# Kernel tuning notes

Hardware: AMD Instinct MI355X
Metric: run time of the kernel (lower is better)

Reference implementation:

```python
import jax, jax.numpy as jnp
import numpy as np

MAX_CH = 21
LAT_DIM = 64
D_EMBED = 1024
N_HEADS = 16
D_HEAD = D_EMBED // N_HEADS  # 64
L = MAX_CH * LAT_DIM         # 1344 latents
B, T = 4, 1024


def setup_inputs() -> dict:
    key = jax.random.key(0)
    k1, k2, k3, k4, k5, k6 = jax.random.split(key, 6)
    x = jax.random.normal(k1, (B, T, D_EMBED), dtype=jnp.float32)
    # boolean channel mask [b, L, T]
    ch_mask = jax.random.randint(k2, (B, L, T), 0, 2) > 0
    # learned latent queries [L, H*d] (xavier-uniform-ish init)
    lim_q = float(np.sqrt(6.0 / (L + N_HEADS * D_HEAD)))
    latent_q = jax.random.uniform(k3, (L, N_HEADS * D_HEAD), minval=-lim_q, maxval=lim_q, dtype=jnp.float32)
    # Linear weights (torch layout: [out, in]) and biases
    lim_w = float(np.sqrt(1.0 / D_EMBED))
    w_k_w = jax.random.uniform(k4, (N_HEADS * D_HEAD, D_EMBED), minval=-lim_w, maxval=lim_w, dtype=jnp.float32)
    w_k_b = jnp.zeros((N_HEADS * D_HEAD,), dtype=jnp.float32)
    w_v_w = jax.random.uniform(k5, (N_HEADS * D_HEAD, D_EMBED), minval=-lim_w, maxval=lim_w, dtype=jnp.float32)
    w_v_b = jax.random.uniform(k6, (N_HEADS * D_HEAD,), minval=-lim_w, maxval=lim_w, dtype=jnp.float32)
    return {"x": x, "ch_mask": ch_mask, "latent_q": latent_q,
            "w_k_w": w_k_w, "w_k_b": w_k_b, "w_v_w": w_v_w, "w_v_b": w_v_b}


def reference(x, ch_mask, latent_q, w_k_w, w_k_b, w_v_w, w_v_b):
    b, t, d = x.shape
    H, dh = N_HEADS, D_HEAD
    l = latent_q.shape[0]
    # faithful to torch .view(-1, H, L, d): raw row-major reinterpretation
    lq = latent_q.reshape(1, H, l, dh)                    # [1,H,L,dh]
    k = (x @ w_k_w.T + w_k_b).reshape(b, t, H, dh).transpose(0, 2, 3, 1)  # [b,H,dh,T]
    v = (x @ w_v_w.T + w_v_b).reshape(b, t, H, dh).transpose(0, 2, 1, 3)  # [b,H,T,dh]
    scale = jnp.float32(H) ** -0.5  # note: n_heads**-0.5, as in source
    scores = jnp.einsum('ohld,bhdt->bhlt', lq, k) * scale  # [b,H,L,T]
    mask = ch_mask[:, None, :, :]                           # [b,1,L,T] broadcast over heads
    scores = jnp.where(mask, scores, jnp.float32(-1e9))
    w = jax.nn.softmax(scores, axis=-1)
    w = jnp.where(mask, w, jnp.float32(0.0))
    out = jnp.einsum('bhlt,bhtd->bhld', w, v)               # [b,H,L,dh]
    return out.transpose(0, 2, 1, 3).reshape(b, l, H * dh)  # [b,L,H*dh]
```

## Files before the change

### kernel.cpp

```cpp
#include <hip/hip_runtime.h>
#include <hip/hip_bf16.h>

#define B_SZ 4
#define T_SZ 1024
#define NH 16
#define L_SZ 1344
#define LT_COUNT 21

typedef __attribute__((ext_vector_type(8))) short short8;
typedef __attribute__((ext_vector_type(4))) short short4v;
typedef __attribute__((ext_vector_type(4))) float floatx4;

typedef __attribute__((address_space(1))) const void gvoid;
typedef __attribute__((address_space(3))) void svoid;
#define GLD16(gp, lp) \
  __builtin_amdgcn_global_load_lds((gvoid*)(gp), (svoid*)(lp), 16, 0, 0)

static __device__ inline short bf16bits(float f) {
  return __builtin_bit_cast(short, __float2bfloat16(f));
}
static __device__ inline short4v cvt4(float4 v) {
  short4v r;
  r.x = bf16bits(v.x); r.y = bf16bits(v.y);
  r.z = bf16bits(v.z); r.w = bf16bits(v.w);
  return r;
}

static __device__ inline void store_kv(int gn, int grow, float val,
    __hip_bfloat16* __restrict__ k_buf, __hip_bfloat16* __restrict__ v_buf) {
  int b = grow >> 10, t = grow & 1023;
  if (gn < 1024) {
    int h = gn >> 6, d = gn & 63;
    int bh = b * 16 + h;
    int tc = t >> 6, ni = (t >> 4) & 3, c15 = t & 15;
    int half = (d >> 5) & 1, q4 = (d >> 3) & 3, jj = d & 7;
    k_buf[(size_t)((bh * 16 + tc) * 8 + ni * 2 + half) * 512 +
          (q4 * 16 + c15) * 8 + jj] = __float2bfloat16(val);
  } else {
    int dd = gn - 1024;
    int h = dd >> 6, d = dd & 63;
    int bh = b * 16 + h;
    int tc = t >> 6, half = (t >> 5) & 1, q4 = (t >> 3) & 3, jj = t & 7;
    int di = (d >> 4) & 3, c15 = d & 15;
    v_buf[(size_t)((bh * 16 + tc) * 8 + di * 2 + half) * 512 +
          (q4 * 16 + c15) * 8 + jj] = __float2bfloat16(val);
  }
}

__global__ __launch_bounds__(256) void mask_detect(
    const unsigned char* __restrict__ m, int* __restrict__ flag) {
  __shared__ int any_off4, any_at4;
  if (threadIdx.x == 0) { any_off4 = 0; any_at4 = 0; }
  __syncthreads();
  int a1 = 0, a2 = 0;
  for (int i = threadIdx.x; i < 8192; i += 256) {
    unsigned char v = m[i];
    if (v) {
      if ((i & 3) != 0) a1 = 1;
      if ((i & 7) == 4) a2 = 1;
    }
  }
  if (a1) atomicOr(&any_off4, 1);
  if (a2) atomicOr(&any_at4, 1);
  __syncthreads();
  if (threadIdx.x == 0) *flag = any_off4 ? 1 : (any_at4 ? 0 : 2);
}

__global__ __launch_bounds__(256) void maskbits_kernel(
    const void* __restrict__ mask, const int* __restrict__ flag,
    unsigned int* __restrict__ bits) {
  int idx = blockIdx.x * 256 + threadIdx.x;
  int f = *flag;
  bool v;
  if (f == 1)      v = ((const signed char*)mask)[idx] != 0;
  else if (f == 2) v = ((const long long*)mask)[idx] != 0;
  else             v = ((const int*)mask)[idx] != 0;
  unsigned long long bal = __ballot(v);
  int lane = threadIdx.x & 63;
  if ((lane & 31) == 0) {
    unsigned int w = (lane & 32) ? (unsigned int)(bal >> 32) : (unsigned int)bal;
    bits[idx >> 5] = w;
  }
}

__global__ __launch_bounds__(256) void cvt_bf16(
    const float4* __restrict__ src, short4v* __restrict__ dst) {
  size_t i = (size_t)blockIdx.x * 256 + threadIdx.x;
  dst[i] = cvt4(src[i]);
}

__global__ __launch_bounds__(256) void kv_gemm_bf16(
    const __hip_bfloat16* __restrict__ xb,
    const __hip_bfloat16* __restrict__ wb,
    const float* __restrict__ bk, const float* __restrict__ bv,
    __hip_bfloat16* __restrict__ k_buf, __hip_bfloat16* __restrict__ v_buf) {
  __shared__ __align__(16) __hip_bfloat16 ldsA[128 * 32];
  __shared__ __align__(16) __hip_bfloat16 ldsB[128 * 32];

  const int tid = threadIdx.x, lane = tid & 63, w = tid >> 6;
  const int wm = w & 1, wn = w >> 1;
  const int bx = blockIdx.x, by = blockIdx.y;
  const int c15 = lane & 15, kq = lane >> 4;

  floatx4 acc[4][4];
  for (int i = 0; i < 4; ++i)
    for (int j = 0; j < 4; ++j) acc[i][j] = (floatx4){0.f, 0.f, 0.f, 0.f};

  for (int kk = 0; kk < 1024; kk += 32) {
    #pragma unroll
    for (int j = 0; j < 2; ++j) {
      int c = w * 128 + j * 64 + lane;
      int row = c >> 2;
      int gkc = (c & 3) ^ (row & 3);
      GLD16(xb + (size_t)(by * 128 + row) * 1024 + kk + gkc * 8,
            ldsA + (w * 128 + j * 64) * 8);
      GLD16(wb + (size_t)(bx * 128 + row) * 1024 + kk + gkc * 8,
            ldsB + (w * 128 + j * 64) * 8);
    }
    __syncthreads();

    short8 af[4], bf[4];
    #pragma unroll
    for (int mi = 0; mi < 4; ++mi) {
      int row = wm * 64 + mi * 16 + c15;
      af[mi] = *(const short8*)(ldsA + row * 32 + ((kq ^ (row & 3)) * 8));
    }
    #pragma unroll
    for (int ni = 0; ni < 4; ++ni) {
      int row = wn * 64 + ni * 16 + c15;
      bf[ni] = *(const short8*)(ldsB + row * 32 + ((kq ^ (row & 3)) * 8));
    }
    #pragma unroll
    for (int mi = 0; mi < 4; ++mi)
      #pragma unroll
      for (int ni = 0; ni < 4; ++ni)
        acc[mi][ni] = __builtin_amdgcn_mfma_f32_16x16x32_bf16(af[mi], bf[ni], acc[mi][ni], 0, 0, 0);
    __syncthreads();
  }

  #pragma unroll
  for (int ni = 0; ni < 4; ++ni) {
    int gn = bx * 128 + wn * 64 + ni * 16 + c15;
    float bias = (gn < 1024) ? bk[gn] : bv[gn - 1024];
    #pragma unroll
    for (int mi = 0; mi < 4; ++mi) {
      int grow0 = by * 128 + wm * 64 + mi * 16 + (kq << 2);
      #pragma unroll
      for (int r = 0; r < 4; ++r)
        store_kv(gn, grow0 + r, acc[mi][ni][r] + bias, k_buf, v_buf);
    }
  }
}

__global__ __launch_bounds__(256) void kv_gemm_f32(
    const float* __restrict__ x,
    const float* __restrict__ wk, const float* __restrict__ bk,
    const float* __restrict__ wv, const float* __restrict__ bv,
    __hip_bfloat16* __restrict__ k_buf, __hip_bfloat16* __restrict__ v_buf) {
  __shared__ __align__(16) __hip_bfloat16 ldsA[128 * 40];
  __shared__ __align__(16) __hip_bfloat16 ldsB[128 * 40];
  const int tid = threadIdx.x, lane = tid & 63, w = tid >> 6;
  const int wm = w & 1, wn = w >> 1;
  const int bx = blockIdx.x, by = blockIdx.y;
  const bool isK = (bx < 8);
  const float* W = isK ? wk : wv;
  const int n0 = bx * 128 - (isK ? 0 : 1024);
  floatx4 acc[4][4];
  for (int i = 0; i < 4; ++i)
    for (int j = 0; j < 4; ++j) acc[i][j] = (floatx4){0.f, 0.f, 0.f, 0.f};
  const int c15 = lane & 15, kq = lane >> 4;
  for (int kk = 0; kk < 1024; kk += 32) {
    #pragma unroll
    for (int j = 0; j < 4; ++j) {
      int f = tid + 256 * j;
      int row = f >> 3, c4 = (f & 7) * 4;
      float4 va = *(const float4*)(x + (size_t)(by * 128 + row) * 1024 + kk + c4);
      float4 vb = *(const float4*)(W + (size_t)(n0 + row) * 1024 + kk + c4);
      *(short4v*)(ldsA + row * 40 + c4) = cvt4(va);
      *(short4v*)(ldsB + row * 40 + c4) = cvt4(vb);
    }
    __syncthreads();
    short8 af[4], bf[4];
    #pragma unroll
    for (int mi = 0; mi < 4; ++mi)
      af[mi] = *(const short8*)(ldsA + (wm * 64 + mi * 16 + c15) * 40 + kq * 8);
    #pragma unroll
    for (int ni = 0; ni < 4; ++ni)
      bf[ni] = *(const short8*)(ldsB + (wn * 64 + ni * 16 + c15) * 40 + kq * 8);
    #pragma unroll
    for (int mi = 0; mi < 4; ++mi)
      #pragma unroll
      for (int ni = 0; ni < 4; ++ni)
        acc[mi][ni] = __builtin_amdgcn_mfma_f32_16x16x32_bf16(af[mi], bf[ni], acc[mi][ni], 0, 0, 0);
    __syncthreads();
  }
  #pragma unroll
  for (int ni = 0; ni < 4; ++ni) {
    int gn = bx * 128 + wn * 64 + ni * 16 + c15;
    float bias = (gn < 1024) ? bk[gn] : bv[gn - 1024];
    #pragma unroll
    for (int mi = 0; mi < 4; ++mi) {
      int grow0 = by * 128 + wm * 64 + mi * 16 + (kq << 2);
      #pragma unroll
      for (int r = 0; r < 4; ++r)
        store_kv(gn, grow0 + r, acc[mi][ni][r] + bias, k_buf, v_buf);
    }
  }
}

__global__ __launch_bounds__(64, 4) void attn_kernel(
    const float* __restrict__ latent_q,
    const __hip_bfloat16* __restrict__ k_buf,
    const __hip_bfloat16* __restrict__ v_buf,
    const unsigned int* __restrict__ mbits,
    float* __restrict__ out) {
  __shared__ __align__(16) __hip_bfloat16 pbuf[2][16 * 72];

  const int lane = threadIdx.x & 63;
  int bid = blockIdx.x;
  int xcd = bid & 7, j = bid >> 3;
  int bh = xcd * 8 + j / 84;
  int r84 = j % 84;
  int lt = r84 >> 2, sub = r84 & 3;
  int h = bh & 15, b = bh >> 4;
  const int q4 = lane >> 4, c15 = lane & 15;
  const int l = lt * 64 + sub * 16 + c15;

  const float QS = 0.25f * 1.44269504089f;
  short8 qf[2];
  {
    const float* qp = latent_q + ((size_t)(h * L_SZ + l)) * 64 + q4 * 8;
    float4 a0 = *(const float4*)(qp);
    float4 a1 = *(const float4*)(qp + 4);
    float4 a2 = *(const float4*)(qp + 32);
    float4 a3 = *(const float4*)(qp + 36);
    a0.x *= QS; a0.y *= QS; a0.z *= QS; a0.w *= QS;
    a1.x *= QS; a1.y *= QS; a1.z *= QS; a1.w *= QS;
    a2.x *= QS; a2.y *= QS; a2.z *= QS; a2.w *= QS;
    a3.x *= QS; a3.y *= QS; a3.z *= QS; a3.w *= QS;
    short4v l0 = cvt4(a0), l1 = cvt4(a1), l2 = cvt4(a2), l3 = cvt4(a3);
    qf[0] = (short8){l0.x, l0.y, l0.z, l0.w, l1.x, l1.y, l1.z, l1.w};
    qf[1] = (short8){l2.x, l2.y, l2.z, l2.w, l3.x, l3.y, l3.z, l3.w};
  }

  float l_acc = 0.f;
  floatx4 o_acc[4];
  #pragma unroll
  for (int di = 0; di < 4; ++di) o_acc[di] = (floatx4){0.f, 0.f, 0.f, 0.f};

  const __hip_bfloat16* kb = k_buf + (size_t)bh * 16 * 4096;
  const __hip_bfloat16* vb = v_buf + (size_t)bh * 16 * 4096;
  const unsigned int* mrow = mbits + ((size_t)(b * L_SZ + l)) * 32;

  for (int tc = 0; tc < 16; ++tc) {
    short8 kf[2][4];
    #pragma unroll
    for (int half = 0; half < 2; ++half)
      #pragma unroll
      for (int ni = 0; ni < 4; ++ni)
        kf[half][ni] = *(const short8*)(kb + (size_t)(tc * 8 + ni * 2 + half) * 512 + lane * 8);
    uint2 mw = *(const uint2*)(mrow + tc * 2);

    floatx4 s[4];
    #pragma unroll
    for (int ni = 0; ni < 4; ++ni) s[ni] = (floatx4){0.f, 0.f, 0.f, 0.f};
    #pragma unroll
    for (int half = 0; half < 2; ++half)
      #pragma unroll
      for (int ni = 0; ni < 4; ++ni)
        s[ni] = __builtin_amdgcn_mfma_f32_16x16x32_bf16(kf[half][ni], qf[half], s[ni], 0, 0, 0);

    short8 vf[2][4];
    #pragma unroll
    for (int half = 0; half < 2; ++half)
      #pragma unroll
      for (int di = 0; di < 4; ++di)
        vf[half][di] = *(const short8*)(vb + (size_t)(tc * 8 + di * 2 + half) * 512 + lane * 8);

    __hip_bfloat16* pw = pbuf[tc & 1];
    #pragma unroll
    for (int ni = 0; ni < 4; ++ni) {
      unsigned mword = (ni >= 2) ? mw.y : mw.x;
      float4 p4;
      #pragma unroll
      for (int r = 0; r < 4; ++r) {
        float e = exp2f(s[ni][r]);
        int sh = (ni & 1) * 16 + q4 * 4 + r;
        float pv = ((mword >> sh) & 1) ? e : 0.f;
        l_acc += pv;
        ((float*)&p4)[r] = pv;
      }
      *(short4v*)(pw + c15 * 72 + ni * 16 + q4 * 4) = cvt4(p4);
    }

    short8 pf0 = *(const short8*)(pw + c15 * 72 + q4 * 8);
    short8 pf1 = *(const short8*)(pw + c15 * 72 + 32 + q4 * 8);

    #pragma unroll
    for (int di = 0; di < 4; ++di)
      o_acc[di] = __builtin_amdgcn_mfma_f32_16x16x32_bf16(vf[0][di], pf0, o_acc[di], 0, 0, 0);
    #pragma unroll
    for (int di = 0; di < 4; ++di)
      o_acc[di] = __builtin_amdgcn_mfma_f32_16x16x32_bf16(vf[1][di], pf1, o_acc[di], 0, 0, 0);
  }

  l_acc += __shfl_xor(l_acc, 16, 64);
  l_acc += __shfl_xor(l_acc, 32, 64);
  float inv = (l_acc > 0.f) ? 1.f / l_acc : 0.f;
  float* ob = out + ((size_t)(b * L_SZ + l)) * 1024 + h * 64;
  #pragma unroll
  for (int di = 0; di < 4; ++di) {
    float4 o4 = {o_acc[di][0] * inv, o_acc[di][1] * inv,
                 o_acc[di][2] * inv, o_acc[di][3] * inv};
    *(float4*)(ob + di * 16 + q4 * 4) = o4;
  }
}

extern "C" void kernel_launch(void* const* d_in, const int* in_sizes, int n_in,
                              void* d_out, int out_size, void* d_ws, size_t ws_size,
                              hipStream_t stream) {
  const float* x      = (const float*)d_in[0];
  const void* ch_mask = d_in[1];
  const float* lq     = (const float*)d_in[2];
  const float* wk     = (const float*)d_in[3];
  const float* bk     = (const float*)d_in[4];
  const float* wv     = (const float*)d_in[5];
  const float* bv     = (const float*)d_in[6];
  float* out = (float*)d_out;

  char* ws = (char*)d_ws;
  unsigned int* mbits   = (unsigned int*)ws;
  int* flag             = (int*)(ws + (992u * 1024));
  __hip_bfloat16* k_buf = (__hip_bfloat16*)(ws + (1u << 20));
  __hip_bfloat16* v_buf = (__hip_bfloat16*)(ws + (9u << 20));
  __hip_bfloat16* xb    = (__hip_bfloat16*)(ws + (17u << 20));
  __hip_bfloat16* wb    = (__hip_bfloat16*)(ws + (25u << 20));

  mask_detect<<<1, 256, 0, stream>>>((const unsigned char*)ch_mask, flag);
  maskbits_kernel<<<21504, 256, 0, stream>>>(ch_mask, flag, mbits);

  if (ws_size >= (30u << 20)) {
    cvt_bf16<<<4096, 256, 0, stream>>>((const float4*)x, (short4v*)xb);
    cvt_bf16<<<1024, 256, 0, stream>>>((const float4*)wk, (short4v*)wb);
    cvt_bf16<<<1024, 256, 0, stream>>>((const float4*)wv,
                                       (short4v*)(wb + 1024 * 1024));
    kv_gemm_bf16<<<dim3(16, 32), 256, 0, stream>>>(xb, wb, bk, bv, k_buf, v_buf);
  } else {
    kv_gemm_f32<<<dim3(16, 32), 256, 0, stream>>>(x, wk, bk, wv, bv, k_buf, v_buf);
  }

  attn_kernel<<<8 * 672, 64, 0, stream>>>(lq, k_buf, v_buf, mbits, out);
}
```

Baseline: 218.4 us.

## Process 64 latents per attention wave and split K/V GEMMs with vectorized epilogues

The attention kernel now handles four 16-latent groups per wavefront, so each K/V fragment load from global memory serves four score/PV MFMA sets. The mask words for the tile are staged in LDS up front. The fused KV GEMM is split into separate K and V GEMMs. K is computed transposed (W·xᵀ) so the epilogue writes contiguous 4-element bf16 vectors in the swizzled layout instead of scattered scalar stores. The trade-off is higher register pressure (launch bounds drop to 2 waves), a quarter as many attention blocks, and one more kernel launch.

```diff
diff --git a/kernel.cpp b/kernel.cpp
--- a/kernel.cpp
+++ b/kernel.cpp
@@ -26,26 +26,6 @@
   return r;
 }
 
-static __device__ inline void store_kv(int gn, int grow, float val,
-    __hip_bfloat16* __restrict__ k_buf, __hip_bfloat16* __restrict__ v_buf) {
-  int b = grow >> 10, t = grow & 1023;
-  if (gn < 1024) {
-    int h = gn >> 6, d = gn & 63;
-    int bh = b * 16 + h;
-    int tc = t >> 6, ni = (t >> 4) & 3, c15 = t & 15;
-    int half = (d >> 5) & 1, q4 = (d >> 3) & 3, jj = d & 7;
-    k_buf[(size_t)((bh * 16 + tc) * 8 + ni * 2 + half) * 512 +
-          (q4 * 16 + c15) * 8 + jj] = __float2bfloat16(val);
-  } else {
-    int dd = gn - 1024;
-    int h = dd >> 6, d = dd & 63;
-    int bh = b * 16 + h;
-    int tc = t >> 6, half = (t >> 5) & 1, q4 = (t >> 3) & 3, jj = t & 7;
-    int di = (d >> 4) & 3, c15 = d & 15;
-    v_buf[(size_t)((bh * 16 + tc) * 8 + di * 2 + half) * 512 +
-          (q4 * 16 + c15) * 8 + jj] = __float2bfloat16(val);
-  }
-}
 
 __global__ __launch_bounds__(256) void mask_detect(
     const unsigned char* __restrict__ m, int* __restrict__ flag) {
@@ -89,147 +69,193 @@
   dst[i] = cvt4(src[i]);
 }
 
-__global__ __launch_bounds__(256) void kv_gemm_bf16(
-    const __hip_bfloat16* __restrict__ xb,
-    const __hip_bfloat16* __restrict__ wb,
-    const float* __restrict__ bk, const float* __restrict__ bv,
-    __hip_bfloat16* __restrict__ k_buf, __hip_bfloat16* __restrict__ v_buf) {
-  __shared__ __align__(16) __hip_bfloat16 ldsA[128 * 32];
-  __shared__ __align__(16) __hip_bfloat16 ldsB[128 * 32];
-
-  const int tid = threadIdx.x, lane = tid & 63, w = tid >> 6;
-  const int wm = w & 1, wn = w >> 1;
-  const int bx = blockIdx.x, by = blockIdx.y;
-  const int c15 = lane & 15, kq = lane >> 4;
-
-  floatx4 acc[4][4];
-  for (int i = 0; i < 4; ++i)
-    for (int j = 0; j < 4; ++j) acc[i][j] = (floatx4){0.f, 0.f, 0.f, 0.f};
-
-  for (int kk = 0; kk < 1024; kk += 32) {
-    #pragma unroll
-    for (int j = 0; j < 2; ++j) {
-      int c = w * 128 + j * 64 + lane;
-      int row = c >> 2;
-      int gkc = (c & 3) ^ (row & 3);
-      GLD16(xb + (size_t)(by * 128 + row) * 1024 + kk + gkc * 8,
-            ldsA + (w * 128 + j * 64) * 8);
-      GLD16(wb + (size_t)(bx * 128 + row) * 1024 + kk + gkc * 8,
-            ldsB + (w * 128 + j * 64) * 8);
-    }
-    __syncthreads();
-
-    short8 af[4], bf[4];
+static __device__ inline void epi_k(const floatx4 acc[4][4],
+    int bx, int by, int wm, int wn, int c15, int kq,
+    const float* __restrict__ bk, __hip_bfloat16* __restrict__ k_buf) {
+  #pragma unroll
+  for (int ni = 0; ni < 4; ++ni) {
+    int gr = bx * 128 + wn * 64 + ni * 16 + c15;
+    int b = gr >> 10, tc = (gr >> 6) & 15;
     #pragma unroll
     for (int mi = 0; mi < 4; ++mi) {
-      int row = wm * 64 + mi * 16 + c15;
-      af[mi] = *(const short8*)(ldsA + row * 32 + ((kq ^ (row & 3)) * 8));
-    }
-    #pragma unroll
-    for (int ni = 0; ni < 4; ++ni) {
-      int row = wn * 64 + ni * 16 + c15;
-      bf[ni] = *(const short8*)(ldsB + row * 32 + ((kq ^ (row & 3)) * 8));
-    }
-    #pragma unroll
-    for (int mi = 0; mi < 4; ++mi)
-      #pragma unroll
-      for (int ni = 0; ni < 4; ++ni)
-        acc[mi][ni] = __builtin_amdgcn_mfma_f32_16x16x32_bf16(af[mi], bf[ni], acc[mi][ni], 0, 0, 0);
-    __syncthreads();
-  }
-
+      int d0 = by * 128 + wm * 64 + mi * 16 + kq * 4;
+      int h = d0 >> 6, hd = d0 & 63;
+      int half = hd >> 5, q4 = (hd >> 3) & 3, jlo = hd & 7;
+      int bh = b * 16 + h;
+      float4 b4 = *(const float4*)(bk + d0);
+      float4 v4 = {acc[mi][ni][0] + b4.x, acc[mi][ni][1] + b4.y,
+                   acc[mi][ni][2] + b4.z, acc[mi][ni][3] + b4.w};
+      *(short4v*)(k_buf + ((size_t)((bh * 16 + tc) * 8 + ni * 2 + half)) * 512 +
+                  (q4 * 16 + c15) * 8 + jlo) = cvt4(v4);
+    }
+  }
+}
+
+static __device__ inline void epi_v(const floatx4 acc[4][4],
+    int bx, int by, int wm, int wn, int c15, int kq,
+    const float* __restrict__ bv, __hip_bfloat16* __restrict__ v_buf) {
   #pragma unroll
   for (int ni = 0; ni < 4; ++ni) {
-    int gn = bx * 128 + wn * 64 + ni * 16 + c15;
-    float bias = (gn < 1024) ? bk[gn] : bv[gn - 1024];
+    int d = bx * 128 + wn * 64 + ni * 16 + c15;
+    int h = d >> 6;
+    float bias = bv[d];
     #pragma unroll
     for (int mi = 0; mi < 4; ++mi) {
-      int grow0 = by * 128 + wm * 64 + mi * 16 + (kq << 2);
-      #pragma unroll
-      for (int r = 0; r < 4; ++r)
-        store_kv(gn, grow0 + r, acc[mi][ni][r] + bias, k_buf, v_buf);
-    }
-  }
-}
-
-__global__ __launch_bounds__(256) void kv_gemm_f32(
-    const float* __restrict__ x,
-    const float* __restrict__ wk, const float* __restrict__ bk,
-    const float* __restrict__ wv, const float* __restrict__ bv,
-    __hip_bfloat16* __restrict__ k_buf, __hip_bfloat16* __restrict__ v_buf) {
-  __shared__ __align__(16) __hip_bfloat16 ldsA[128 * 40];
-  __shared__ __align__(16) __hip_bfloat16 ldsB[128 * 40];
-  const int tid = threadIdx.x, lane = tid & 63, w = tid >> 6;
-  const int wm = w & 1, wn = w >> 1;
-  const int bx = blockIdx.x, by = blockIdx.y;
-  const bool isK = (bx < 8);
-  const float* W = isK ? wk : wv;
-  const int n0 = bx * 128 - (isK ? 0 : 1024);
-  floatx4 acc[4][4];
-  for (int i = 0; i < 4; ++i)
-    for (int j = 0; j < 4; ++j) acc[i][j] = (floatx4){0.f, 0.f, 0.f, 0.f};
-  const int c15 = lane & 15, kq = lane >> 4;
-  for (int kk = 0; kk < 1024; kk += 32) {
-    #pragma unroll
-    for (int j = 0; j < 4; ++j) {
-      int f = tid + 256 * j;
-      int row = f >> 3, c4 = (f & 7) * 4;
-      float4 va = *(const float4*)(x + (size_t)(by * 128 + row) * 1024 + kk + c4);
-      float4 vb = *(const float4*)(W + (size_t)(n0 + row) * 1024 + kk + c4);
-      *(short4v*)(ldsA + row * 40 + c4) = cvt4(va);
-      *(short4v*)(ldsB + row * 40 + c4) = cvt4(vb);
-    }
-    __syncthreads();
-    short8 af[4], bf[4];
-    #pragma unroll
-    for (int mi = 0; mi < 4; ++mi)
-      af[mi] = *(const short8*)(ldsA + (wm * 64 + mi * 16 + c15) * 40 + kq * 8);
-    #pragma unroll
-    for (int ni = 0; ni < 4; ++ni)
-      bf[ni] = *(const short8*)(ldsB + (wn * 64 + ni * 16 + c15) * 40 + kq * 8);
-    #pragma unroll
-    for (int mi = 0; mi < 4; ++mi)
-      #pragma unroll
-      for (int ni = 0; ni < 4; ++ni)
-        acc[mi][ni] = __builtin_amdgcn_mfma_f32_16x16x32_bf16(af[mi], bf[ni], acc[mi][ni], 0, 0, 0);
-    __syncthreads();
-  }
-  #pragma unroll
-  for (int ni = 0; ni < 4; ++ni) {
-    int gn = bx * 128 + wn * 64 + ni * 16 + c15;
-    float bias = (gn < 1024) ? bk[gn] : bv[gn - 1024];
-    #pragma unroll
-    for (int mi = 0; mi < 4; ++mi) {
-      int grow0 = by * 128 + wm * 64 + mi * 16 + (kq << 2);
-      #pragma unroll
-      for (int r = 0; r < 4; ++r)
-        store_kv(gn, grow0 + r, acc[mi][ni][r] + bias, k_buf, v_buf);
-    }
-  }
-}
-
-__global__ __launch_bounds__(64, 4) void attn_kernel(
+      int gr = by * 128 + wm * 64 + mi * 16 + kq * 4;
+      int b = gr >> 10, tc = (gr >> 6) & 15;
+      int tl = gr & 63;
+      int half = tl >> 5, q4 = (tl >> 3) & 3, jlo = tl & 7;
+      int bh = b * 16 + h;
+      float4 v4 = {acc[mi][ni][0] + bias, acc[mi][ni][1] + bias,
+                   acc[mi][ni][2] + bias, acc[mi][ni][3] + bias};
+      *(short4v*)(v_buf + ((size_t)((bh * 16 + tc) * 8 + ni * 2 + half)) * 512 +
+                  (q4 * 16 + c15) * 8 + jlo) = cvt4(v4);
+    }
+  }
+}
+
+#define GEMM_BF16_CORE(Abase, Bbase)                                          \
+  __shared__ __align__(16) __hip_bfloat16 ldsA[128 * 32];                     \
+  __shared__ __align__(16) __hip_bfloat16 ldsB[128 * 32];                     \
+  const int tid = threadIdx.x, lane = tid & 63, w = tid >> 6;                 \
+  const int wm = w & 1, wn = w >> 1;                                          \
+  const int bx = blockIdx.x, by = blockIdx.y;                                 \
+  const int c15 = lane & 15, kq = lane >> 4;                                  \
+  floatx4 acc[4][4];                                                          \
+  for (int i = 0; i < 4; ++i)                                                 \
+    for (int j = 0; j < 4; ++j) acc[i][j] = (floatx4){0.f, 0.f, 0.f, 0.f};    \
+  for (int kk = 0; kk < 1024; kk += 32) {                                     \
+    _Pragma("unroll")                                                         \
+    for (int j = 0; j < 2; ++j) {                                             \
+      int c = w * 128 + j * 64 + lane;                                        \
+      int row = c >> 2;                                                       \
+      int gkc = (c & 3) ^ (row & 3);                                          \
+      GLD16(Abase + (size_t)(by * 128 + row) * 1024 + kk + gkc * 8,           \
+            ldsA + (w * 128 + j * 64) * 8);                                   \
+      GLD16(Bbase + (size_t)(bx * 128 + row) * 1024 + kk + gkc * 8,           \
+            ldsB + (w * 128 + j * 64) * 8);                                   \
+    }                                                                         \
+    __syncthreads();                                                          \
+    short8 af[4], bf[4];                                                      \
+    _Pragma("unroll")                                                         \
+    for (int mi = 0; mi < 4; ++mi) {                                          \
+      int row = wm * 64 + mi * 16 + c15;                                      \
+      af[mi] = *(const short8*)(ldsA + row * 32 + ((kq ^ (row & 3)) * 8));    \
+    }                                                                         \
+    _Pragma("unroll")                                                         \
+    for (int ni = 0; ni < 4; ++ni) {                                          \
+      int row = wn * 64 + ni * 16 + c15;                                      \
+      bf[ni] = *(const short8*)(ldsB + row * 32 + ((kq ^ (row & 3)) * 8));    \
+    }                                                                         \
+    _Pragma("unroll")                                                         \
+    for (int mi = 0; mi < 4; ++mi)                                            \
+      _Pragma("unroll")                                                       \
+      for (int ni = 0; ni < 4; ++ni)                                          \
+        acc[mi][ni] = __builtin_amdgcn_mfma_f32_16x16x32_bf16(                \
+            af[mi], bf[ni], acc[mi][ni], 0, 0, 0);                            \
+    __syncthreads();                                                          \
+  }
+
+__global__ __launch_bounds__(256) void gemm_k_bf16(
+    const __hip_bfloat16* __restrict__ wkb, const __hip_bfloat16* __restrict__ xb,
+    const float* __restrict__ bk, __hip_bfloat16* __restrict__ k_buf) {
+  GEMM_BF16_CORE(wkb, xb)
+  epi_k(acc, bx, by, wm, wn, c15, kq, bk, k_buf);
+}
+
+__global__ __launch_bounds__(256) void gemm_v_bf16(
+    const __hip_bfloat16* __restrict__ xb, const __hip_bfloat16* __restrict__ wvb,
+    const float* __restrict__ bv, __hip_bfloat16* __restrict__ v_buf) {
+  GEMM_BF16_CORE(xb, wvb)
+  epi_v(acc, bx, by, wm, wn, c15, kq, bv, v_buf);
+}
+
+#define GEMM_F32_CORE(Abase, Bbase)                                           \
+  __shared__ __align__(16) __hip_bfloat16 ldsA[128 * 40];                     \
+  __shared__ __align__(16) __hip_bfloat16 ldsB[128 * 40];                     \
+  const int tid = threadIdx.x, lane = tid & 63, w = tid >> 6;                 \
+  const int wm = w & 1, wn = w >> 1;                                          \
+  const int bx = blockIdx.x, by = blockIdx.y;                                 \
+  const int c15 = lane & 15, kq = lane >> 4;                                  \
+  floatx4 acc[4][4];                                                          \
+  for (int i = 0; i < 4; ++i)                                                 \
+    for (int j = 0; j < 4; ++j) acc[i][j] = (floatx4){0.f, 0.f, 0.f, 0.f};    \
+  for (int kk = 0; kk < 1024; kk += 32) {                                     \
+    _Pragma("unroll")                                                         \
+    for (int j = 0; j < 4; ++j) {                                             \
+      int f = tid + 256 * j;                                                  \
+      int row = f >> 3, c4 = (f & 7) * 4;                                     \
+      float4 va = *(const float4*)(Abase + (size_t)(by * 128 + row) * 1024 + kk + c4); \
+      float4 vb = *(const float4*)(Bbase + (size_t)(bx * 128 + row) * 1024 + kk + c4); \
+      *(short4v*)(ldsA + row * 40 + c4) = cvt4(va);                           \
+      *(short4v*)(ldsB + row * 40 + c4) = cvt4(vb);                           \
+    }                                                                         \
+    __syncthreads();                                                          \
+    short8 af[4], bf[4];                                                      \
+    _Pragma("unroll")                                                         \
+    for (int mi = 0; mi < 4; ++mi)                                            \
+      af[mi] = *(const short8*)(ldsA + (wm * 64 + mi * 16 + c15) * 40 + kq * 8); \
+    _Pragma("unroll")                                                         \
+    for (int ni = 0; ni < 4; ++ni)                                            \
+      bf[ni] = *(const short8*)(ldsB + (wn * 64 + ni * 16 + c15) * 40 + kq * 8); \
+    _Pragma("unroll")                                                         \
+    for (int mi = 0; mi < 4; ++mi)                                            \
+      _Pragma("unroll")                                                       \
+      for (int ni = 0; ni < 4; ++ni)                                          \
+        acc[mi][ni] = __builtin_amdgcn_mfma_f32_16x16x32_bf16(                \
+            af[mi], bf[ni], acc[mi][ni], 0, 0, 0);                            \
+    __syncthreads();                                                          \
+  }
+
+__global__ __launch_bounds__(256) void gemm_k_f32(
+    const float* __restrict__ wk, const float* __restrict__ x,
+    const float* __restrict__ bk, __hip_bfloat16* __restrict__ k_buf) {
+  GEMM_F32_CORE(wk, x)
+  epi_k(acc, bx, by, wm, wn, c15, kq, bk, k_buf);
+}
+
+__global__ __launch_bounds__(256) void gemm_v_f32(
+    const float* __restrict__ x, const float* __restrict__ wv,
+    const float* __restrict__ bv, __hip_bfloat16* __restrict__ v_buf) {
+  GEMM_F32_CORE(x, wv)
+  epi_v(acc, bx, by, wm, wn, c15, kq, bv, v_buf);
+}
+
+__global__ __launch_bounds__(64, 2) void attn_kernel(
     const float* __restrict__ latent_q,
     const __hip_bfloat16* __restrict__ k_buf,
     const __hip_bfloat16* __restrict__ v_buf,
     const unsigned int* __restrict__ mbits,
     float* __restrict__ out) {
-  __shared__ __align__(16) __hip_bfloat16 pbuf[2][16 * 72];
+  __shared__ __align__(16) __hip_bfloat16 pbuf[4][16 * 72];
+  __shared__ uint2 mrows[64][17];
 
   const int lane = threadIdx.x & 63;
   int bid = blockIdx.x;
   int xcd = bid & 7, j = bid >> 3;
-  int bh = xcd * 8 + j / 84;
-  int r84 = j % 84;
-  int lt = r84 >> 2, sub = r84 & 3;
+  int bh = xcd * 8 + j / LT_COUNT;
+  int lt = j % LT_COUNT;
   int h = bh & 15, b = bh >> 4;
   const int q4 = lane >> 4, c15 = lane & 15;
-  const int l = lt * 64 + sub * 16 + c15;
+  const int l0 = lt * 64;
+
+  {
+    const unsigned int* msrc = mbits + (size_t)(b * L_SZ + l0) * 32;
+    #pragma unroll
+    for (int p = 0; p < 8; ++p) {
+      int i = p * 64 + lane;
+      uint4 m4 = *(const uint4*)(msrc + i * 4);
+      int row = i >> 3, c2 = (i & 7) * 2;
+      mrows[row][c2]     = make_uint2(m4.x, m4.y);
+      mrows[row][c2 + 1] = make_uint2(m4.z, m4.w);
+    }
+  }
 
   const float QS = 0.25f * 1.44269504089f;
-  short8 qf[2];
-  {
-    const float* qp = latent_q + ((size_t)(h * L_SZ + l)) * 64 + q4 * 8;
+  short8 qf[4][2];
+  #pragma unroll
+  for (int g = 0; g < 4; ++g) {
+    const float* qp = latent_q + ((size_t)(h * L_SZ + l0 + g * 16 + c15)) * 64 + q4 * 8;
     float4 a0 = *(const float4*)(qp);
     float4 a1 = *(const float4*)(qp + 4);
     float4 a2 = *(const float4*)(qp + 32);
@@ -238,81 +264,88 @@
     a1.x *= QS; a1.y *= QS; a1.z *= QS; a1.w *= QS;
     a2.x *= QS; a2.y *= QS; a2.z *= QS; a2.w *= QS;
     a3.x *= QS; a3.y *= QS; a3.z *= QS; a3.w *= QS;
-    short4v l0 = cvt4(a0), l1 = cvt4(a1), l2 = cvt4(a2), l3 = cvt4(a3);
-    qf[0] = (short8){l0.x, l0.y, l0.z, l0.w, l1.x, l1.y, l1.z, l1.w};
-    qf[1] = (short8){l2.x, l2.y, l2.z, l2.w, l3.x, l3.y, l3.z, l3.w};
-  }
-
-  float l_acc = 0.f;
-  floatx4 o_acc[4];
-  #pragma unroll
-  for (int di = 0; di < 4; ++di) o_acc[di] = (floatx4){0.f, 0.f, 0.f, 0.f};
-
-  const __hip_bfloat16* kb = k_buf + (size_t)bh * 16 * 4096;
-  const __hip_bfloat16* vb = v_buf + (size_t)bh * 16 * 4096;
-  const unsigned int* mrow = mbits + ((size_t)(b * L_SZ + l)) * 32;
+    short4v t0 = cvt4(a0), t1 = cvt4(a1), t2 = cvt4(a2), t3 = cvt4(a3);
+    qf[g][0] = (short8){t0.x, t0.y, t0.z, t0.w, t1.x, t1.y, t1.z, t1.w};
+    qf[g][1] = (short8){t2.x, t2.y, t2.z, t2.w, t3.x, t3.y, t3.z, t3.w};
+  }
+
+  float l_acc[4] = {0.f, 0.f, 0.f, 0.f};
+  floatx4 o_acc[4][4];
+  #pragma unroll
+  for (int g = 0; g < 4; ++g)
+    #pragma unroll
+    for (int di = 0; di < 4; ++di) o_acc[g][di] = (floatx4){0.f, 0.f, 0.f, 0.f};
+
+  const __hip_bfloat16* kb = k_buf + (size_t)bh * 65536;
+  const __hip_bfloat16* vb = v_buf + (size_t)bh * 65536;
 
   for (int tc = 0; tc < 16; ++tc) {
-    short8 kf[2][4];
+    short8 kf[2][4], vf[2][4];
     #pragma unroll
     for (int half = 0; half < 2; ++half)
       #pragma unroll
       for (int ni = 0; ni < 4; ++ni)
         kf[half][ni] = *(const short8*)(kb + (size_t)(tc * 8 + ni * 2 + half) * 512 + lane * 8);
-    uint2 mw = *(const uint2*)(mrow + tc * 2);
-
-    floatx4 s[4];
-    #pragma unroll
-    for (int ni = 0; ni < 4; ++ni) s[ni] = (floatx4){0.f, 0.f, 0.f, 0.f};
-    #pragma unroll
-    for (int half = 0; half < 2; ++half)
-      #pragma unroll
-      for (int ni = 0; ni < 4; ++ni)
-        s[ni] = __builtin_amdgcn_mfma_f32_16x16x32_bf16(kf[half][ni], qf[half], s[ni], 0, 0, 0);
-
-    short8 vf[2][4];
     #pragma unroll
     for (int half = 0; half < 2; ++half)
       #pragma unroll
       for (int di = 0; di < 4; ++di)
         vf[half][di] = *(const short8*)(vb + (size_t)(tc * 8 + di * 2 + half) * 512 + lane * 8);
 
-    __hip_bfloat16* pw = pbuf[tc & 1];
-    #pragma unroll
-    for (int ni = 0; ni < 4; ++ni) {
-      unsigned mword = (ni >= 2) ? mw.y : mw.x;
-      float4 p4;
-      #pragma unroll
-      for (int r = 0; r < 4; ++r) {
-        float e = exp2f(s[ni][r]);
-        int sh = (ni & 1) * 16 + q4 * 4 + r;
-        float pv = ((mword >> sh) & 1) ? e : 0.f;
-        l_acc += pv;
-        ((float*)&p4)[r] = pv;
+    #pragma unroll
+    for (int g = 0; g < 4; ++g) {
+      uint2 mw = mrows[g * 16 + c15][tc];
+      floatx4 s[4];
+      #pragma unroll
+      for (int ni = 0; ni < 4; ++ni) s[ni] = (floatx4){0.f, 0.f, 0.f, 0.f};
+      #pragma unroll
+      for (int half = 0; half < 2; ++half)
+        #pragma unroll
+        for (int ni = 0; ni < 4; ++ni)
+          s[ni] = __builtin_amdgcn_mfma_f32_16x16x32_bf16(kf[half][ni], qf[g][half], s[ni], 0, 0, 0);
+      __hip_bfloat16* pw = pbuf[g];
+      #pragma unroll
+      for (int ni = 0; ni < 4; ++ni) {
+        unsigned mword = (ni >= 2) ? mw.y : mw.x;
+        float4 p4;
+        #pragma unroll
+        for (int r = 0; r < 4; ++r) {
+          float e = exp2f(s[ni][r]);
+          int sh = (ni & 1) * 16 + q4 * 4 + r;
+          float pv = ((mword >> sh) & 1) ? e : 0.f;
+          l_acc[g] += pv;
+          ((float*)&p4)[r] = pv;
+        }
+        *(short4v*)(pw + c15 * 72 + ni * 16 + q4 * 4) = cvt4(p4);
       }
-      *(short4v*)(pw + c15 * 72 + ni * 16 + q4 * 4) = cvt4(p4);
-    }
-
-    short8 pf0 = *(const short8*)(pw + c15 * 72 + q4 * 8);
-    short8 pf1 = *(const short8*)(pw + c15 * 72 + 32 + q4 * 8);
-
-    #pragma unroll
-    for (int di = 0; di < 4; ++di)
-      o_acc[di] = __builtin_amdgcn_mfma_f32_16x16x32_bf16(vf[0][di], pf0, o_acc[di], 0, 0, 0);
-    #pragma unroll
-    for (int di = 0; di < 4; ++di)
-      o_acc[di] = __builtin_amdgcn_mfma_f32_16x16x32_bf16(vf[1][di], pf1, o_acc[di], 0, 0, 0);
-  }
-
-  l_acc += __shfl_xor(l_acc, 16, 64);
-  l_acc += __shfl_xor(l_acc, 32, 64);
-  float inv = (l_acc > 0.f) ? 1.f / l_acc : 0.f;
-  float* ob = out + ((size_t)(b * L_SZ + l)) * 1024 + h * 64;
-  #pragma unroll
-  for (int di = 0; di < 4; ++di) {
-    float4 o4 = {o_acc[di][0] * inv, o_acc[di][1] * inv,
-                 o_acc[di][2] * inv, o_acc[di][3] * inv};
-    *(float4*)(ob + di * 16 + q4 * 4) = o4;
+    }
+
+    #pragma unroll
+    for (int g = 0; g < 4; ++g) {
+      short8 pf0 = *(const short8*)(pbuf[g] + c15 * 72 + q4 * 8);
+      short8 pf1 = *(const short8*)(pbuf[g] + c15 * 72 + 32 + q4 * 8);
+      #pragma unroll
+      for (int di = 0; di < 4; ++di)
+        o_acc[g][di] = __builtin_amdgcn_mfma_f32_16x16x32_bf16(vf[0][di], pf0, o_acc[g][di], 0, 0, 0);
+      #pragma unroll
+      for (int di = 0; di < 4; ++di)
+        o_acc[g][di] = __builtin_amdgcn_mfma_f32_16x16x32_bf16(vf[1][di], pf1, o_acc[g][di], 0, 0, 0);
+    }
+  }
+
+  #pragma unroll
+  for (int g = 0; g < 4; ++g) {
+    float la = l_acc[g];
+    la += __shfl_xor(la, 16, 64);
+    la += __shfl_xor(la, 32, 64);
+    float inv = (la > 0.f) ? 1.f / la : 0.f;
+    float* ob = out + ((size_t)(b * L_SZ + l0 + g * 16 + c15)) * 1024 + h * 64;
+    #pragma unroll
+    for (int di = 0; di < 4; ++di) {
+      float4 o4 = {o_acc[g][di][0] * inv, o_acc[g][di][1] * inv,
+                   o_acc[g][di][2] * inv, o_acc[g][di][3] * inv};
+      *(float4*)(ob + di * 16 + q4 * 4) = o4;
+    }
   }
 }
 
@@ -334,20 +367,22 @@
   __hip_bfloat16* k_buf = (__hip_bfloat16*)(ws + (1u << 20));
   __hip_bfloat16* v_buf = (__hip_bfloat16*)(ws + (9u << 20));
   __hip_bfloat16* xb    = (__hip_bfloat16*)(ws + (17u << 20));
-  __hip_bfloat16* wb    = (__hip_bfloat16*)(ws + (25u << 20));
+  __hip_bfloat16* wkb   = (__hip_bfloat16*)(ws + (25u << 20));
+  __hip_bfloat16* wvb   = (__hip_bfloat16*)(ws + (27u << 20));
 
   mask_detect<<<1, 256, 0, stream>>>((const unsigned char*)ch_mask, flag);
   maskbits_kernel<<<21504, 256, 0, stream>>>(ch_mask, flag, mbits);
 
   if (ws_size >= (30u << 20)) {
     cvt_bf16<<<4096, 256, 0, stream>>>((const float4*)x, (short4v*)xb);
-    cvt_bf16<<<1024, 256, 0, stream>>>((const float4*)wk, (short4v*)wb);
-    cvt_bf16<<<1024, 256, 0, stream>>>((const float4*)wv,
-                                       (short4v*)(wb + 1024 * 1024));
-    kv_gemm_bf16<<<dim3(16, 32), 256, 0, stream>>>(xb, wb, bk, bv, k_buf, v_buf);
+    cvt_bf16<<<1024, 256, 0, stream>>>((const float4*)wk, (short4v*)wkb);
+    cvt_bf16<<<1024, 256, 0, stream>>>((const float4*)wv, (short4v*)wvb);
+    gemm_k_bf16<<<dim3(32, 8), 256, 0, stream>>>(wkb, xb, bk, k_buf);
+    gemm_v_bf16<<<dim3(8, 32), 256, 0, stream>>>(xb, wvb, bv, v_buf);
   } else {
-    kv_gemm_f32<<<dim3(16, 32), 256, 0, stream>>>(x, wk, bk, wv, bv, k_buf, v_buf);
-  }
-
-  attn_kernel<<<8 * 672, 64, 0, stream>>>(lq, k_buf, v_buf, mbits, out);
-}
+    gemm_k_f32<<<dim3(32, 8), 256, 0, stream>>>(wk, x, bk, k_buf);
+    gemm_v_f32<<<dim3(8, 32), 256, 0, stream>>>(x, wv, bv, v_buf);
+  }
+
+  attn_kernel<<<8 * 168, 64, 0, stream>>>(lq, k_buf, v_buf, mbits, out);
+}
```

New measurement: 229.8 us. +5.2%, slower.
